# Kernel tuning notes

Measured on AMD Instinct MI355X. Metric: run time of the kernel, lower is better.

Reference implementation:

```python
import jax, jax.numpy as jnp
import numpy as np

K = 3  # kernel_dim
PAD = 1


def setup_inputs() -> dict:
    key = jax.random.key(0)
    ks = jax.random.split(key, 7)
    B, C_in, C_out, R = 2, 32, 64, 64
    H = W = D = 64
    return {
        "x": jax.random.normal(ks[0], (B, C_in, H, W, D), dtype=jnp.float32),
        "U_k_h": jax.random.normal(ks[1], (K, R), dtype=jnp.float32),
        "U_k_w": jax.random.normal(ks[2], (K, R), dtype=jnp.float32),
        "U_k_d": jax.random.normal(ks[3], (K, R), dtype=jnp.float32),
        "U_c_in": jax.random.normal(ks[4], (C_in, R), dtype=jnp.float32),
        "U_c_out": jax.random.normal(ks[5], (R, C_out), dtype=jnp.float32),
        "bias": jax.random.normal(ks[6], (C_out,), dtype=jnp.float32),
    }


def _cpd_conv3d(x, U_k_h, U_k_w, U_k_d, U_c_in, U_c_out, bias):
    # Equivalent to: patches[b,c,h,w,d,kh,kw,kd] contracted with
    # U_c_in[c,r] U_k_h[kh,r] U_k_w[kw,r] U_k_d[kd,r] U_c_out[r,co]
    # -> out[b,co,h,w,d].  We exploit the CP (rank-separable) structure
    # instead of materializing the unfolded patch tensor.
    xp = jnp.pad(x, ((0, 0), (0, 0), (PAD, PAD), (PAD, PAD), (PAD, PAD)))
    # channel contraction: [B, R, H+2, W+2, D+2]
    t = jnp.einsum('bchwd,cr->brhwd', xp, U_c_in)
    B, R, Hp, Wp, Dp = t.shape
    H, W, D = Hp - 2 * PAD, Wp - 2 * PAD, Dp - 2 * PAD
    # separable kernel contractions (fixed K=3 unrolled loops)
    t = sum(t[:, :, k:k + H, :, :] * U_k_h[k][None, :, None, None, None] for k in range(K))
    t = sum(t[:, :, :, k:k + W, :] * U_k_w[k][None, :, None, None, None] for k in range(K))
    t = sum(t[:, :, :, :, k:k + D] * U_k_d[k][None, :, None, None, None] for k in range(K))
    out = jnp.einsum('brhwd,rc->bchwd', t, U_c_out)
    return out + bias[None, :, None, None, None]


def reference(x, U_k_h, U_k_w, U_k_d, U_c_in, U_c_out, bias):
    return _cpd_conv3d(x, U_k_h, U_k_w, U_k_d, U_c_in, U_c_out, bias)
```

## Files before the change

### kernel.cpp

```cpp
#include <hip/hip_runtime.h>
#include <hip/hip_bf16.h>

typedef __attribute__((ext_vector_type(8))) short short8;
typedef __attribute__((ext_vector_type(4))) float f32x4;

__device__ __forceinline__ float b2f(short s) {
    return __uint_as_float(((unsigned int)(unsigned short)s) << 16);
}
__device__ __forceinline__ short f2b(float f) {
    unsigned int u = __float_as_uint(f);
    u += 0x7fffu + ((u >> 16) & 1u);
    return (short)(u >> 16);
}
__device__ __forceinline__ unsigned pack2(float a, float b) {
    return (unsigned)(unsigned short)f2b(a) | ((unsigned)(unsigned short)f2b(b) << 16);
}

__global__ __launch_bounds__(64)
void k0_prep(const float* __restrict__ Uco, const float* __restrict__ Ucin,
             short* __restrict__ ucotT, short* __restrict__ ucinT)
{
    const int i = blockIdx.x * 64 + threadIdx.x;
    if (i < 4096) {
        int co = i >> 6, r = i & 63;
        ucotT[co * 64 + r] = f2b(Uco[r * 64 + co]);
    } else {
        int j = i - 4096;
        int r = j >> 5, c = j & 31;
        ucinT[r * 32 + c] = f2b(Ucin[c * 64 + r]);
    }
}

__global__ __launch_bounds__(256)
void k1_channel(const float* __restrict__ x,
                const float* __restrict__ Ucin,
                const short* __restrict__ ucinT_g,
                short* __restrict__ t)
{
    __shared__ short xs[256 * 32];
    __shared__ short uci[64 * 32];

    const int tid = threadIdx.x;
    const int gp0 = blockIdx.x * 256;
    const int b   = gp0 >> 18;
    const int sp  = (gp0 & 262143) + tid;
    const float* xp = x + ((long)b << 23) + sp;

    if (ucinT_g) {
        ((short8*)uci)[tid] = ((const short8*)ucinT_g)[tid];
    } else {
        for (int i = tid; i < 2048; i += 256) {
            int r = i >> 5, c = i & 31;
            uci[i] = f2b(Ucin[c * 64 + r]);
        }
    }

    {
        float v[32];
#pragma unroll
        for (int c = 0; c < 32; ++c) v[c] = xp[(long)c << 18];
        const int swz = (tid >> 1) & 3;
#pragma unroll
        for (int oct = 0; oct < 4; ++oct) {
            short8 o;
#pragma unroll
            for (int j = 0; j < 8; ++j) o[j] = f2b(v[oct * 8 + j]);
            *(short8*)&xs[tid * 32 + ((oct ^ swz) << 3)] = o;
        }
    }
    __syncthreads();

    const int lane = tid & 63, wv = tid >> 6;
    const int l15 = lane & 15, quad = lane >> 4;

    short8 afr[4];
#pragma unroll
    for (int mt = 0; mt < 4; ++mt)
        afr[mt] = *(const short8*)&uci[(mt * 16 + l15) * 32 + quad * 8];

    f32x4 acc[4][4] = {};
#pragma unroll
    for (int nt = 0; nt < 4; ++nt) {
        const int srow = wv * 64 + nt * 16 + l15;
        const int slot = quad ^ ((srow >> 1) & 3);
        short8 bfr = *(const short8*)&xs[srow * 32 + (slot << 3)];
#pragma unroll
        for (int mt = 0; mt < 4; ++mt)
            acc[mt][nt] = __builtin_amdgcn_mfma_f32_16x16x32_bf16(
                afr[mt], bfr, acc[mt][nt], 0, 0, 0);
    }

#pragma unroll
    for (int nt = 0; nt < 4; ++nt) {
        const int srow = wv * 64 + nt * 16 + l15;
        short* tb = t + ((size_t)(gp0 + srow) << 6);
#pragma unroll
        for (int mt = 0; mt < 4; ++mt) {
            uint2 o;
            o.x = pack2(acc[mt][nt][0], acc[mt][nt][1]);
            o.y = pack2(acc[mt][nt][2], acc[mt][nt][3]);
            *(uint2*)&tb[mt * 16 + quad * 4] = o;
        }
    }
}

__global__ __launch_bounds__(256)
void k2_conv_gemm(const short* __restrict__ t,
                  const float* __restrict__ Ukh,
                  const float* __restrict__ Ukw,
                  const float* __restrict__ Ukd,
                  const float* __restrict__ Uco,
                  const float* __restrict__ bias,
                  const short* __restrict__ ucotT,
                  float* __restrict__ out)
{
    __shared__ short s[66 * 64];
    __shared__ short p[64 * 72];
    __shared__ short ucot[64 * 72];

    const int tid = threadIdx.x;

    const int bid  = blockIdx.x;
    const int slot = bid & 7;
    const int idx  = bid >> 3;
    const int b    = idx >> 9;
    const int rem  = idx & 511;
    const int h    = slot * 8 + (rem >> 6);
    const int w    = rem & 63;

    const short* colp[9];
    bool valid[9];
#pragma unroll
    for (int kh = 0; kh < 3; ++kh) {
#pragma unroll
        for (int kw = 0; kw < 3; ++kw) {
            int hh = h + kh - 1, ww = w + kw - 1;
            bool v = ((unsigned)hh < 64u) && ((unsigned)ww < 64u);
            valid[kh * 3 + kw] = v;
            long base = v ? ((long)(b * 262144 + hh * 4096 + ww * 64) << 6) : 0;
            colp[kh * 3 + kw] = t + base;
        }
    }

    if (ucotT) {
        for (int i = tid; i < 512; i += 256) {
            int co = i >> 3, rb = i & 7;
            short8 v = *(const short8*)&ucotT[co * 64 + rb * 8];
            *(short8*)&ucot[co * 72 + rb * 8] = v;
        }
    } else {
        for (int i = tid; i < 4096; i += 256) {
            int r = i >> 6, co = i & 63;
            ucot[co * 72 + r] = f2b(Uco[i]);
        }
    }

    const int rq = tid & 15;
    float4 W[9];
    {
        float4 a[3], c[3];
#pragma unroll
        for (int k = 0; k < 3; ++k) {
            a[k] = *(const float4*)&Ukh[k * 64 + 4 * rq];
            c[k] = *(const float4*)&Ukw[k * 64 + 4 * rq];
        }
#pragma unroll
        for (int kh = 0; kh < 3; ++kh)
#pragma unroll
            for (int kw = 0; kw < 3; ++kw) {
                int kk = kh * 3 + kw;
                float m = valid[kk] ? 1.f : 0.f;
                W[kk].x = a[kh].x * c[kw].x * m;
                W[kk].y = a[kh].y * c[kw].y * m;
                W[kk].z = a[kh].z * c[kw].z * m;
                W[kk].w = a[kh].w * c[kw].w * m;
            }
    }

    if (tid < 32) {
        int sd = (tid < 16) ? 0 : 65;
        int rr = tid & 15;
        uint2 z; z.x = 0u; z.y = 0u;
        *(uint2*)&s[sd * 64 + 4 * rr] = z;
    }

    {
        const int off0 = (tid >> 4) * 64 + 4 * rq;
        uint2 cur[9];
#pragma unroll
        for (int kk = 0; kk < 9; ++kk)
            cur[kk] = *(const uint2*)(colp[kk] + off0);

#pragma unroll
        for (int j = 0; j < 4; ++j) {
            uint2 nxt[9];
            if (j < 3) {
#pragma unroll
                for (int kk = 0; kk < 9; ++kk)
                    nxt[kk] = *(const uint2*)(colp[kk] + off0 + 1024 * (j + 1));
            }
            float a0 = 0.f, a1 = 0.f, a2 = 0.f, a3 = 0.f;
#pragma unroll
            for (int kk = 0; kk < 9; ++kk) {
                uint2 uu = cur[kk];
                a0 += W[kk].x * b2f((short)(uu.x));
                a1 += W[kk].y * b2f((short)(uu.x >> 16));
                a2 += W[kk].z * b2f((short)(uu.y));
                a3 += W[kk].w * b2f((short)(uu.y >> 16));
            }
            int sd = 1 + (tid >> 4) + 16 * j;
            uint2 o; o.x = pack2(a0, a1); o.y = pack2(a2, a3);
            *(uint2*)&s[sd * 64 + 4 * rq] = o;
            if (j < 3) {
#pragma unroll
                for (int kk = 0; kk < 9; ++kk) cur[kk] = nxt[kk];
            }
        }
    }
    __syncthreads();

    {
        float4 Wd[3];
#pragma unroll
        for (int k = 0; k < 3; ++k)
            Wd[k] = *(const float4*)&Ukd[k * 64 + 4 * rq];
        for (int u = tid; u < 64 * 16; u += 256) {
            int d = u >> 4;
            float a0 = 0.f, a1 = 0.f, a2 = 0.f, a3 = 0.f;
#pragma unroll
            for (int k = 0; k < 3; ++k) {
                uint2 uu = *(const uint2*)&s[(d + k) * 64 + 4 * rq];
                a0 += Wd[k].x * b2f((short)(uu.x));
                a1 += Wd[k].y * b2f((short)(uu.x >> 16));
                a2 += Wd[k].z * b2f((short)(uu.y));
                a3 += Wd[k].w * b2f((short)(uu.y >> 16));
            }
            uint2 o; o.x = pack2(a0, a1); o.y = pack2(a2, a3);
            *(uint2*)&p[d * 72 + 4 * rq] = o;
        }
    }
    __syncthreads();

    {
        const int lane = tid & 63, wv = tid >> 6;
        const int l15 = lane & 15, quad = lane >> 4;
        short8 afr0 = *(const short8*)&p[(wv * 16 + l15) * 72 + quad * 8];
        short8 afr1 = *(const short8*)&p[(wv * 16 + l15) * 72 + 32 + quad * 8];
        f32x4 acc[4] = {};
#pragma unroll
        for (int nt = 0; nt < 4; ++nt) {
            short8 b0 = *(const short8*)&ucot[(nt * 16 + l15) * 72 + quad * 8];
            short8 b1 = *(const short8*)&ucot[(nt * 16 + l15) * 72 + 32 + quad * 8];
            acc[nt] = __builtin_amdgcn_mfma_f32_16x16x32_bf16(afr0, b0, acc[nt], 0, 0, 0);
            acc[nt] = __builtin_amdgcn_mfma_f32_16x16x32_bf16(afr1, b1, acc[nt], 0, 0, 0);
        }
#pragma unroll
        for (int nt = 0; nt < 4; ++nt) {
            int co = nt * 16 + l15;
            float bs = bias[co];
            int d = wv * 16 + quad * 4;
            float4 o;
            o.x = acc[nt][0] + bs; o.y = acc[nt][1] + bs;
            o.z = acc[nt][2] + bs; o.w = acc[nt][3] + bs;
            long addr = ((long)(b * 64 + co) << 18) + (h << 12) + (w << 6) + d;
            *(float4*)&out[addr] = o;
        }
    }
}

#define NTH 512
#define NPADP 656
#define SMEM_BYTES ((NPADP*32 + NPADP*32 + 432*32 + 64*32 + 64*64)*2 + 576*4)

__global__ __launch_bounds__(NTH)
void cpd_conv3d_fused_fb(const float* __restrict__ x,
                         const float* __restrict__ Ukh,
                         const float* __restrict__ Ukw,
                         const float* __restrict__ Ukd,
                         const float* __restrict__ Ucin,
                         const float* __restrict__ Uco,
                         const float* __restrict__ bias,
                         float* __restrict__ out)
{
    extern __shared__ char smem[];
    short* xs   = (short*)smem;
    short* t0   = xs   + NPADP*32;
    short* t1   = t0   + NPADP*32;
    short* uct  = t1   + 432*32;
    short* ucot = uct  + 64*32;
    float* ukf  = (float*)(ucot + 64*64);

    const int tid  = threadIdx.x;
    const int lane = tid & 63;
    const int wv   = tid >> 6;
    const int l15  = lane & 15;
    const int quad = lane >> 4;
    const int rg   = tid & 3;

    const int bid = blockIdx.x;
    const int dt = bid & 3, wt = (bid >> 2) & 15, ht = (bid >> 6) & 15, b = bid >> 10;
    const int h0 = ht * 4, w0 = wt * 4, d0 = dt * 16;

    for (int i = tid; i < 576; i += NTH) {
        float v = (i < 192) ? Ukh[i] : (i < 384 ? Ukw[i - 192] : Ukd[i - 384]);
        ukf[i] = v;
    }
    for (int i = tid; i < 2048; i += NTH) {
        int r = i >> 5, c = i & 31;
        uct[i] = f2b(Ucin[c * 64 + r]);
    }
    for (int i = tid; i < 4096; i += NTH) {
        int co = i >> 6, r = i & 63;
        ucot[i] = f2b(Uco[r * 64 + co]);
    }
    for (int i = tid; i < NPADP * 32; i += NTH) {
        int pp = i >> 5, c = i & 31;
        float v = 0.f;
        if (pp < 648) {
            int ph = pp / 108, rem = pp - ph * 108;
            int pw = rem / 18, pd = rem - pw * 18;
            int gh = h0 + ph - 1, gw = w0 + pw - 1, gd = d0 + pd - 1;
            if ((unsigned)gh < 64u && (unsigned)gw < 64u && (unsigned)gd < 64u)
                v = x[((long)(b * 32 + c) << 18) + (gh << 12) + (gw << 6) + gd];
        }
        xs[i] = f2b(v);
    }
    __syncthreads();

    f32x4 acc[8] = {};

    for (int pass = 0; pass < 2; ++pass) {
        const int rbase = pass * 32;
        {
            const int nt = wv & 1;
            short8 bfrag = *(const short8*)&uct[(rbase + nt * 16 + l15) * 32 + quad * 8];
            for (int mt = (wv >> 1); mt <= 40; mt += 4) {
                short8 afrag = *(const short8*)&xs[(mt * 16 + l15) * 32 + quad * 8];
                f32x4 c = {};
                c = __builtin_amdgcn_mfma_f32_16x16x32_bf16(afrag, bfrag, c, 0, 0, 0);
                const int col = nt * 16 + l15;
#pragma unroll
                for (int i2 = 0; i2 < 4; ++i2)
                    t0[(mt * 16 + quad * 4 + i2) * 32 + col] = f2b(c[i2]);
            }
        }
        __syncthreads();
        {
            float wh[3][8];
#pragma unroll
            for (int k = 0; k < 3; ++k) {
                const float4* pp_ = (const float4*)&ukf[k * 64 + rbase + rg * 8];
                float4 u0 = pp_[0], u1 = pp_[1];
                wh[k][0]=u0.x; wh[k][1]=u0.y; wh[k][2]=u0.z; wh[k][3]=u0.w;
                wh[k][4]=u1.x; wh[k][5]=u1.y; wh[k][6]=u1.z; wh[k][7]=u1.w;
            }
            for (int item = tid; item < 1728; item += NTH) {
                int q = item >> 2;
                float v[8] = {};
#pragma unroll
                for (int k = 0; k < 3; ++k) {
                    short8 sv = *(const short8*)&t0[(q + k * 108) * 32 + rg * 8];
#pragma unroll
                    for (int j = 0; j < 8; ++j) v[j] += wh[k][j] * b2f(sv[j]);
                }
                short8 o;
#pragma unroll
                for (int j = 0; j < 8; ++j) o[j] = f2b(v[j]);
                *(short8*)&t1[q * 32 + rg * 8] = o;
            }
        }
        __syncthreads();
        {
            float ww[3][8];
#pragma unroll
            for (int k = 0; k < 3; ++k) {
                const float4* pp_ = (const float4*)&ukf[(3 + k) * 64 + rbase + rg * 8];
                float4 u0 = pp_[0], u1 = pp_[1];
                ww[k][0]=u0.x; ww[k][1]=u0.y; ww[k][2]=u0.z; ww[k][3]=u0.w;
                ww[k][4]=u1.x; ww[k][5]=u1.y; ww[k][6]=u1.z; ww[k][7]=u1.w;
            }
            for (int item = tid; item < 1152; item += NTH) {
                int q2 = item >> 2;
                int oh = q2 / 72;
                int src = q2 + oh * 36;
                float v[8] = {};
#pragma unroll
                for (int k = 0; k < 3; ++k) {
                    short8 sv = *(const short8*)&t1[(src + k * 18) * 32 + rg * 8];
#pragma unroll
                    for (int j = 0; j < 8; ++j) v[j] += ww[k][j] * b2f(sv[j]);
                }
                short8 o;
#pragma unroll
                for (int j = 0; j < 8; ++j) o[j] = f2b(v[j]);
                *(short8*)&t0[q2 * 32 + rg * 8] = o;
            }
        }
        __syncthreads();
        {
            float wd[3][8];
#pragma unroll
            for (int k = 0; k < 3; ++k) {
                const float4* pp_ = (const float4*)&ukf[(6 + k) * 64 + rbase + rg * 8];
                float4 u0 = pp_[0], u1 = pp_[1];
                wd[k][0]=u0.x; wd[k][1]=u0.y; wd[k][2]=u0.z; wd[k][3]=u0.w;
                wd[k][4]=u1.x; wd[k][5]=u1.y; wd[k][6]=u1.z; wd[k][7]=u1.w;
            }
            for (int item = tid; item < 1024; item += NTH) {
                int pq = item >> 2;
                int src = pq + (pq >> 4) * 2;
                float v[8] = {};
#pragma unroll
                for (int k = 0; k < 3; ++k) {
                    short8 sv = *(const short8*)&t0[(src + k) * 32 + rg * 8];
#pragma unroll
                    for (int j = 0; j < 8; ++j) v[j] += wd[k][j] * b2f(sv[j]);
                }
                short8 o;
#pragma unroll
                for (int j = 0; j < 8; ++j) o[j] = f2b(v[j]);
                *(short8*)&t1[pq * 32 + rg * 8] = o;
            }
        }
        __syncthreads();
        {
            short8 bfr[4];
#pragma unroll
            for (int nt = 0; nt < 4; ++nt)
                bfr[nt] = *(const short8*)&ucot[(nt * 16 + l15) * 64 + rbase + quad * 8];
#pragma unroll
            for (int i = 0; i < 8; ++i) {
                int mt = wv * 2 + (i >> 2), nt = i & 3;
                short8 afr = *(const short8*)&t1[(mt * 16 + l15) * 32 + quad * 8];
                acc[i] = __builtin_amdgcn_mfma_f32_16x16x32_bf16(afr, bfr[nt], acc[i], 0, 0, 0);
            }
        }
    }

#pragma unroll
    for (int i = 0; i < 8; ++i) {
        int mt = wv * 2 + (i >> 2), nt = i & 3;
        int co = nt * 16 + l15;
        int oh = mt >> 2, ow = mt & 3;
        float bs = bias[co];
        float4 o4;
        o4.x = acc[i][0] + bs; o4.y = acc[i][1] + bs;
        o4.z = acc[i][2] + bs; o4.w = acc[i][3] + bs;
        long addr = ((long)(b * 64 + co) << 18) + ((long)(h0 + oh) << 12)
                  + ((w0 + ow) << 6) + (d0 + quad * 4);
        *(float4*)&out[addr] = o4;
    }
}

extern "C" void kernel_launch(void* const* d_in, const int* in_sizes, int n_in,
                              void* d_out, int out_size, void* d_ws, size_t ws_size,
                              hipStream_t stream) {
    const float* x    = (const float*)d_in[0];
    const float* Ukh  = (const float*)d_in[1];
    const float* Ukw  = (const float*)d_in[2];
    const float* Ukd  = (const float*)d_in[3];
    const float* Ucin = (const float*)d_in[4];
    const float* Uco  = (const float*)d_in[5];
    const float* bias = (const float*)d_in[6];
    float* out = (float*)d_out;

    const size_t needT = (size_t)2 * 262144 * 64 * 2;
    const size_t needM = (4096 + 2048) * 2;
    if (ws_size >= needT) {
        short* t = (short*)d_ws;
        short* ucotT = nullptr;
        short* ucinT = nullptr;
        if (ws_size >= needT + needM) {
            ucotT = (short*)((char*)d_ws + needT);
            ucinT = ucotT + 4096;
            k0_prep<<<96, 64, 0, stream>>>(Uco, Ucin, ucotT, ucinT);
        }
        k1_channel<<<2048, 256, 0, stream>>>(x, Ucin, ucinT, t);
        k2_conv_gemm<<<8192, 256, 0, stream>>>(t, Ukh, Ukw, Ukd, Uco, bias, ucotT, out);
    } else {
        (void)hipFuncSetAttribute((const void*)cpd_conv3d_fused_fb,
                                  hipFuncAttributeMaxDynamicSharedMemorySize,
                                  SMEM_BYTES);
        cpd_conv3d_fused_fb<<<2048, NTH, SMEM_BYTES, stream>>>(
            x, Ukh, Ukw, Ukd, Ucin, Uco, bias, out);
    }
}
```

Baseline: 264.3 us.

## Fold depth-kernel weights into output projection as banded GEMM

Precomputes gk[k][co][r] = Ukd[k,r]*Uco[r,co] in the prep kernel, so the depth convolution and the output channel projection become a single MFMA GEMM over three shifted rows of the (h,w)-reduced tile. The new conv kernel does the h/w 3x3 stencil in registers into a padded LDS tile, then accumulates three shifted-row GEMMs directly into the output. This removes a separate depth-stencil pass and one LDS intermediate, at the cost of tripling the MFMA count for the output GEMM and one extra bf16 rounding of the folded weights.

```diff
diff --git a/kernel.cpp b/kernel.cpp
--- a/kernel.cpp
+++ b/kernel.cpp
@@ -18,16 +18,23 @@
 
 __global__ __launch_bounds__(64)
 void k0_prep(const float* __restrict__ Uco, const float* __restrict__ Ucin,
-             short* __restrict__ ucotT, short* __restrict__ ucinT)
+             const float* __restrict__ Ukd,
+             short* __restrict__ ucotT, short* __restrict__ ucinT,
+             short* __restrict__ gk)
 {
     const int i = blockIdx.x * 64 + threadIdx.x;
     if (i < 4096) {
         int co = i >> 6, r = i & 63;
         ucotT[co * 64 + r] = f2b(Uco[r * 64 + co]);
-    } else {
+    } else if (i < 6144) {
         int j = i - 4096;
         int r = j >> 5, c = j & 31;
         ucinT[r * 32 + c] = f2b(Ucin[c * 64 + r]);
+    } else if (i < 18432) {
+        int j = i - 6144;
+        int k = j >> 12, rem = j & 4095;
+        int co = rem >> 6, r = rem & 63;
+        gk[j] = f2b(Ukd[k * 64 + r] * Uco[r * 64 + co]);
     }
 }
 
@@ -101,6 +108,142 @@
             o.y = pack2(acc[mt][nt][2], acc[mt][nt][3]);
             *(uint2*)&tb[mt * 16 + quad * 4] = o;
         }
+    }
+}
+
+__global__ __launch_bounds__(256)
+void k2_conv_gemm_gk(const short* __restrict__ t,
+                     const float* __restrict__ Ukh,
+                     const float* __restrict__ Ukw,
+                     const float* __restrict__ bias,
+                     const short* __restrict__ gk,
+                     float* __restrict__ out)
+{
+    __shared__ short s[66 * 72];
+
+    const int tid = threadIdx.x;
+
+    const int bid  = blockIdx.x;
+    const int slot = bid & 7;
+    const int idx  = bid >> 3;
+    const int b    = idx >> 9;
+    const int rem  = idx & 511;
+    const int h    = slot * 8 + (rem >> 6);
+    const int w    = rem & 63;
+
+    const int lane = tid & 63, wv = tid >> 6;
+    const int l15 = lane & 15, quad = lane >> 4;
+    const int co  = wv * 16 + l15;
+
+    short8 bfr[3][2];
+#pragma unroll
+    for (int k = 0; k < 3; ++k)
+#pragma unroll
+        for (int rh = 0; rh < 2; ++rh)
+            bfr[k][rh] = *(const short8*)&gk[(k * 64 + co) * 64 + rh * 32 + quad * 8];
+    const float bs = bias[co];
+
+    const short* colp[9];
+    bool valid[9];
+#pragma unroll
+    for (int kh = 0; kh < 3; ++kh) {
+#pragma unroll
+        for (int kw = 0; kw < 3; ++kw) {
+            int hh = h + kh - 1, ww = w + kw - 1;
+            bool v = ((unsigned)hh < 64u) && ((unsigned)ww < 64u);
+            valid[kh * 3 + kw] = v;
+            long base = v ? ((long)(b * 262144 + hh * 4096 + ww * 64) << 6) : 0;
+            colp[kh * 3 + kw] = t + base;
+        }
+    }
+
+    const int rq = tid & 15;
+    float4 W[9];
+    {
+        float4 a[3], c[3];
+#pragma unroll
+        for (int k = 0; k < 3; ++k) {
+            a[k] = *(const float4*)&Ukh[k * 64 + 4 * rq];
+            c[k] = *(const float4*)&Ukw[k * 64 + 4 * rq];
+        }
+#pragma unroll
+        for (int kh = 0; kh < 3; ++kh)
+#pragma unroll
+            for (int kw = 0; kw < 3; ++kw) {
+                int kk = kh * 3 + kw;
+                float m = valid[kk] ? 1.f : 0.f;
+                W[kk].x = a[kh].x * c[kw].x * m;
+                W[kk].y = a[kh].y * c[kw].y * m;
+                W[kk].z = a[kh].z * c[kw].z * m;
+                W[kk].w = a[kh].w * c[kw].w * m;
+            }
+    }
+
+    if (tid < 32) {
+        int sd = (tid < 16) ? 0 : 65;
+        int rr = tid & 15;
+        uint2 z; z.x = 0u; z.y = 0u;
+        *(uint2*)&s[sd * 72 + 4 * rr] = z;
+    }
+
+    {
+        const int off0 = (tid >> 4) * 64 + 4 * rq;
+        uint2 cur[9];
+#pragma unroll
+        for (int kk = 0; kk < 9; ++kk)
+            cur[kk] = *(const uint2*)(colp[kk] + off0);
+
+#pragma unroll
+        for (int j = 0; j < 4; ++j) {
+            uint2 nxt[9];
+            if (j < 3) {
+#pragma unroll
+                for (int kk = 0; kk < 9; ++kk)
+                    nxt[kk] = *(const uint2*)(colp[kk] + off0 + 1024 * (j + 1));
+            }
+            float a0 = 0.f, a1 = 0.f, a2 = 0.f, a3 = 0.f;
+#pragma unroll
+            for (int kk = 0; kk < 9; ++kk) {
+                uint2 uu = cur[kk];
+                a0 += W[kk].x * b2f((short)(uu.x));
+                a1 += W[kk].y * b2f((short)(uu.x >> 16));
+                a2 += W[kk].z * b2f((short)(uu.y));
+                a3 += W[kk].w * b2f((short)(uu.y >> 16));
+            }
+            int sd = 1 + (tid >> 4) + 16 * j;
+            uint2 o; o.x = pack2(a0, a1); o.y = pack2(a2, a3);
+            *(uint2*)&s[sd * 72 + 4 * rq] = o;
+            if (j < 3) {
+#pragma unroll
+                for (int kk = 0; kk < 9; ++kk) cur[kk] = nxt[kk];
+            }
+        }
+    }
+    __syncthreads();
+
+    f32x4 acc[4] = {};
+#pragma unroll
+    for (int mt = 0; mt < 4; ++mt) {
+#pragma unroll
+        for (int k = 0; k < 3; ++k) {
+            const int row = mt * 16 + l15 + k;
+#pragma unroll
+            for (int rh = 0; rh < 2; ++rh) {
+                short8 afr = *(const short8*)&s[row * 72 + rh * 32 + quad * 8];
+                acc[mt] = __builtin_amdgcn_mfma_f32_16x16x32_bf16(
+                    afr, bfr[k][rh], acc[mt], 0, 0, 0);
+            }
+        }
+    }
+
+#pragma unroll
+    for (int mt = 0; mt < 4; ++mt) {
+        int d = mt * 16 + quad * 4;
+        float4 o;
+        o.x = acc[mt][0] + bs; o.y = acc[mt][1] + bs;
+        o.z = acc[mt][2] + bs; o.w = acc[mt][3] + bs;
+        long addr = ((long)(b * 64 + co) << 18) + (h << 12) + (w << 6) + d;
+        *(float4*)&out[addr] = o;
     }
 }
 
@@ -119,7 +262,6 @@
     __shared__ short ucot[64 * 72];
 
     const int tid = threadIdx.x;
-
     const int bid  = blockIdx.x;
     const int slot = bid & 7;
     const int idx  = bid >> 3;
@@ -465,18 +607,19 @@
     float* out = (float*)d_out;
 
     const size_t needT = (size_t)2 * 262144 * 64 * 2;
-    const size_t needM = (4096 + 2048) * 2;
-    if (ws_size >= needT) {
+    const size_t needM = (4096 + 2048 + 12288) * 2;
+    if (ws_size >= needT + needM) {
+        short* t     = (short*)d_ws;
+        short* ucotT = (short*)((char*)d_ws + needT);
+        short* ucinT = ucotT + 4096;
+        short* gk    = ucinT + 2048;
+        k0_prep<<<288, 64, 0, stream>>>(Uco, Ucin, Ukd, ucotT, ucinT, gk);
+        k1_channel<<<2048, 256, 0, stream>>>(x, Ucin, ucinT, t);
+        k2_conv_gemm_gk<<<8192, 256, 0, stream>>>(t, Ukh, Ukw, bias, gk, out);
+    } else if (ws_size >= needT) {
         short* t = (short*)d_ws;
-        short* ucotT = nullptr;
-        short* ucinT = nullptr;
-        if (ws_size >= needT + needM) {
-            ucotT = (short*)((char*)d_ws + needT);
-            ucinT = ucotT + 4096;
-            k0_prep<<<96, 64, 0, stream>>>(Uco, Ucin, ucotT, ucinT);
-        }
-        k1_channel<<<2048, 256, 0, stream>>>(x, Ucin, ucinT, t);
-        k2_conv_gemm<<<8192, 256, 0, stream>>>(t, Ukh, Ukw, Ukd, Uco, bias, ucotT, out);
+        k1_channel<<<2048, 256, 0, stream>>>(x, Ucin, nullptr, t);
+        k2_conv_gemm<<<8192, 256, 0, stream>>>(t, Ukh, Ukw, Ukd, Uco, bias, nullptr, out);
     } else {
         (void)hipFuncSetAttribute((const void*)cpd_conv3d_fused_fb,
                                   hipFuncAttributeMaxDynamicSharedMemorySize,
```

New measurement: 278.2 us. +5.2%, slower.
